# Performance work log

Hardware: AMD Instinct MI355X
Metric: run time of the kernel (lower is better)

Reference implementation:

```python
import jax, jax.numpy as jnp
import numpy as np

B, T, E, H, C = 64, 512, 512, 1024, 32
FORGET_BIAS = 1.0


def setup_inputs() -> dict:
    key = jax.random.key(0)
    ks = jax.random.split(key, 6)
    x = jax.random.normal(ks[0], (B, T, E), dtype=jnp.float32)
    # one-hot labels (softmax_cross_entropy_with_logits expects a distribution)
    y_idx = jax.random.randint(ks[1], (B,), 0, C)
    y = jax.nn.one_hot(y_idx, C, dtype=jnp.float32)
    seqlen = jnp.full((B,), T, dtype=jnp.int32)  # unused by dynamic_rnn in source
    # BasicLSTMCell kernel: concat([x, h]) @ W + b, gates split as i, j, f, o
    W = jax.random.normal(ks[2], (E + H, 4 * H), dtype=jnp.float32) * 0.02
    b = jnp.zeros((4 * H,), dtype=jnp.float32)
    out_W = jax.random.normal(ks[3], (H, C), dtype=jnp.float32)
    out_b = jax.random.normal(ks[4], (C,), dtype=jnp.float32)
    return {"x": x, "y": y, "seqlen": seqlen, "W": W, "b": b,
            "out_W": out_W, "out_b": out_b}


def lstm_last_output(x, W, b):
    # x: [B, T, E]; returns h_T: [B, H] (== outputs[:, -1] of dynamic_rnn)
    Bn = x.shape[0]
    Hn = W.shape[1] // 4

    def step(carry, xt):
        c, h = carry
        gates = jnp.concatenate([xt, h], axis=1) @ W + b  # [B, 4H]
        i, j, f, o = jnp.split(gates, 4, axis=1)
        new_c = c * jax.nn.sigmoid(f + FORGET_BIAS) + jax.nn.sigmoid(i) * jnp.tanh(j)
        new_h = jnp.tanh(new_c) * jax.nn.sigmoid(o)
        return (new_c, new_h), None

    init = (jnp.zeros((Bn, Hn), x.dtype), jnp.zeros((Bn, Hn), x.dtype))
    (_, h_last), _ = jax.lax.scan(step, init, jnp.swapaxes(x, 0, 1))  # scan over T
    return h_last


def reference(x, y, seqlen, W, b, out_W, out_b):
    h_last = lstm_last_output(x, W, b)
    pred = h_last @ out_W + out_b                    # logits [B, C]
    pred_softmax = jax.nn.softmax(pred, axis=-1)
    log_p = jax.nn.log_softmax(pred, axis=-1)
    cost = jnp.mean(-jnp.sum(y * log_p, axis=-1))    # mean softmax CE
    return pred, pred_softmax, cost
```

## Files before the change

### kernel.cpp

```cpp
#include <hip/hip_runtime.h>
#include <hip/hip_bf16.h>


#define Bb 64
#define Tt 512
#define Ee 512
#define Hh 1024
#define Cc 32
#define G4 4096
#define NKS 48
#define NBLK 128
#define HIDB 8
#define FPAD 32
#define NREP 16

typedef __attribute__((ext_vector_type(8))) short short8;
typedef __attribute__((ext_vector_type(4))) float f32x4;

__device__ __forceinline__ unsigned short f2bf(float f) {
  __hip_bfloat16 h = __float2bfloat16(f);
  union { __hip_bfloat16 h; unsigned short u; } cv; cv.h = h; return cv.u;
}
static __device__ __forceinline__ float fsig(float x) { return 1.0f / (1.0f + __expf(-x)); }
static __device__ __forceinline__ float ftanhf(float x) {
  float e = __expf(-2.0f * fabsf(x));
  float t = (1.0f - e) / (1.0f + e);
  return copysignf(t, x);
}

__global__ __launch_bounds__(256) void transpose_x_kernel(const float* __restrict__ x,
                                                          unsigned short* __restrict__ xT) {
  const int bid = blockIdx.x;
  const int row = bid >> 9, t = bid & (Tt - 1);
  const int e = threadIdx.x * 2;
  const float* src = x + ((size_t)row * Tt + t) * Ee + e;
  float2 v = *(const float2*)src;
  ushort2 o; o.x = f2bf(v.x); o.y = f2bf(v.y);
  *(ushort2*)(xT + ((size_t)t * Bb + row) * Ee + e) = o;
}

__global__ __launch_bounds__(64) void pack_w_kernel(const float* __restrict__ W,
                                                    unsigned short* __restrict__ Wpk) {
  const int fid = blockIdx.x;
  const int l = threadIdx.x;
  const int blk = fid / 96, rem = fid % 96;
  const int tau = rem / 48, ks = rem % 48;
  const int c = l & 15;
  const int col = (2 * tau + (c >> 3)) * Hh + blk * HIDB + (c & 7);
  const int k0 = ks * 32 + (l >> 4) * 8;
  short8 v;
#pragma unroll
  for (int i = 0; i < 8; i++) v[i] = (short)f2bf(W[(size_t)(k0 + i) * G4 + col]);
  *(short8*)(Wpk + ((size_t)fid * 64 + l) * 8) = v;
}

__global__ __launch_bounds__(256) void init_state_kernel(unsigned short* __restrict__ h0,
                                                         int* __restrict__ flg) {
  int i = blockIdx.x * 256 + threadIdx.x;
  h0[i] = 0;
  if (i < 4 * NBLK * FPAD + 4 * NREP * FPAD) flg[i] = 0;
}

__global__ __launch_bounds__(256, 1) void lstm_persist(
    const unsigned short* __restrict__ xT, const unsigned short* __restrict__ Wpk,
    const float* __restrict__ bias,
    unsigned short* __restrict__ hseq,
    float* __restrict__ h_f32, int* __restrict__ flg) {
  const int bc = blockIdx.x;
  const int tid = threadIdx.x;
  const int wv = tid >> 6, ln = tid & 63;

  int* epoch = flg + 4 * NBLK * FPAD;

  if (bc == NBLK) {
    int* flgw2 = flg + wv * NBLK * FPAD;
    int* ep = epoch + wv * NREP * FPAD;
    int cur = 0;
    while (cur < Tt - 1) {
      int a = __hip_atomic_load(flgw2 + ln * FPAD,        __ATOMIC_RELAXED, __HIP_MEMORY_SCOPE_AGENT);
      int b = __hip_atomic_load(flgw2 + (ln + 64) * FPAD, __ATOMIC_RELAXED, __HIP_MEMORY_SCOPE_AGENT);
      int m = a < b ? a : b;
#pragma unroll
      for (int off = 32; off >= 1; off >>= 1) {
        int o = __shfl_xor(m, off);
        m = o < m ? o : m;
      }
      if (m > cur) {
        cur = m;
        if (ln < NREP)
          __hip_atomic_store(ep + ln * FPAD, cur, __ATOMIC_RELAXED, __HIP_MEMORY_SCOPE_AGENT);
      }
    }
    return;
  }

  __shared__ short8 Wl[2 * NKS * 64];

  {
    const short8* src = (const short8*)Wpk + (size_t)bc * (2 * NKS * 64);
    for (int i = tid; i < 2 * NKS * 64; i += 256) Wl[i] = src[i];
  }

  const int c = ln & 15, kg = ln >> 4;
  const int arow = wv * 16 + c;
  const int rbase = wv * 16 + kg * 4;
  const int hid = bc * HIDB + (c & 7);
  const bool lo = (c < 8);
  const float bi = bias[hid], bj = bias[Hh + hid];
  const float bff = bias[2 * Hh + hid], bo = bias[3 * Hh + hid];
  float cstate[4] = {0.f, 0.f, 0.f, 0.f};

  __syncthreads();

  const short8* W0 = Wl;
  const short8* W1 = Wl + NKS * 64;

  short8 wx0[16], wx1[16];
#pragma unroll
  for (int kk = 0; kk < 16; kk++) { wx0[kk] = W0[kk * 64 + ln]; wx1[kk] = W1[kk * 64 + ln]; }

  int* flgw = flg + wv * NBLK * FPAD;
  int* myslot = flgw + bc * FPAD;
  int* myep = epoch + (wv * NREP + (bc & (NREP - 1))) * FPAD;

  f32x4 xa0, xa1;
  {
    const unsigned short* xr = xT + ((size_t)0 * Bb + arow) * Ee + kg * 8;
    f32x4 a0 = {0.f,0.f,0.f,0.f}, a1 = {0.f,0.f,0.f,0.f};
#pragma unroll
    for (int kk = 0; kk < 16; kk++) {
      short8 a = *(const short8*)(xr + kk * 32);
      a0 = __builtin_amdgcn_mfma_f32_16x16x32_bf16(a, wx0[kk], a0, 0, 0, 0);
      a1 = __builtin_amdgcn_mfma_f32_16x16x32_bf16(a, wx1[kk], a1, 0, 0, 0);
    }
    xa0 = a0; xa1 = a1;
  }

  for (int t = 0; t < Tt; t++) {
    while (__hip_atomic_load(myep, __ATOMIC_RELAXED, __HIP_MEMORY_SCOPE_AGENT) < t) { }
    asm volatile("" ::: "memory");

    const unsigned short* hr = hseq + (size_t)t * (NBLK * Bb * HIDB) + kg * 512 + arow * 8;
    short8 f[32];
#pragma unroll
    for (int kk = 0; kk < 32; kk++) f[kk] = *(const short8*)(hr + kk * 2048);
    asm volatile("s_waitcnt vmcnt(16)" ::: "memory");
    __builtin_amdgcn_sched_barrier(0);

    f32x4 a0 = xa0, a1 = xa1;
#pragma unroll
    for (int kk = 0; kk < 16; kk++) {
      a0 = __builtin_amdgcn_mfma_f32_16x16x32_bf16(f[kk], W0[(16 + kk) * 64 + ln], a0, 0, 0, 0);
      a1 = __builtin_amdgcn_mfma_f32_16x16x32_bf16(f[kk], W1[(16 + kk) * 64 + ln], a1, 0, 0, 0);
    }
    asm volatile("s_waitcnt vmcnt(0)" ::: "memory");
    __builtin_amdgcn_sched_barrier(0);
#pragma unroll
    for (int kk = 16; kk < 32; kk++) {
      a0 = __builtin_amdgcn_mfma_f32_16x16x32_bf16(f[kk], W0[(16 + kk) * 64 + ln], a0, 0, 0, 0);
      a1 = __builtin_amdgcn_mfma_f32_16x16x32_bf16(f[kk], W1[(16 + kk) * 64 + ln], a1, 0, 0, 0);
    }

    if (t < Tt - 1) {
      unsigned long long* hob = (unsigned long long*)hseq
                                + (size_t)(t + 1) * (NBLK * Bb * HIDB / 4)
                                + bc * (Bb * HIDB / 4);
#pragma unroll
      for (int r = 0; r < 4; r++) {
        const float p0 = a0[r], p1 = a1[r];
        const float s0 = __shfl_xor(p0, 8), s1 = __shfl_xor(p1, 8);
        const float gi = (lo ? p0 : s0) + bi;
        const float gj = (lo ? s0 : p0) + bj;
        const float gf = (lo ? p1 : s1) + bff;
        const float go = (lo ? s1 : p1) + bo;
        const float cn = cstate[r] * fsig(gf + 1.0f) + fsig(gi) * ftanhf(gj);
        cstate[r] = cn;
        const float hn = ftanhf(cn) * fsig(go);
        unsigned short us = f2bf(hn);
        unsigned short ps = (unsigned short)__shfl_xor((int)us, 1);
        unsigned int hw = (unsigned)us | ((unsigned)ps << 16);
        unsigned int p2 = (unsigned)__shfl_xor((int)hw, 2);
        unsigned long long hq = (unsigned long long)hw | ((unsigned long long)p2 << 32);
        if (lo && !(c & 3))
          __hip_atomic_store(hob + (rbase + r) * 2 + (c >> 2),
                             hq, __ATOMIC_RELAXED, __HIP_MEMORY_SCOPE_AGENT);
      }
      asm volatile("" ::: "memory");
      const unsigned short* xr = xT + ((size_t)(t + 1) * Bb + arow) * Ee + kg * 8;
      short8 xl[16];
#pragma unroll
      for (int kk = 0; kk < 16; kk++) xl[kk] = *(const short8*)(xr + kk * 32);
      asm volatile("s_waitcnt vmcnt(16)" ::: "memory");
      __builtin_amdgcn_sched_barrier(0);
      if (ln == 0)
        __hip_atomic_store(myslot, t + 1, __ATOMIC_RELAXED, __HIP_MEMORY_SCOPE_AGENT);
      {
        f32x4 b0 = {0.f,0.f,0.f,0.f}, b1 = {0.f,0.f,0.f,0.f};
#pragma unroll
        for (int kk = 0; kk < 16; kk++) {
          b0 = __builtin_amdgcn_mfma_f32_16x16x32_bf16(xl[kk], wx0[kk], b0, 0, 0, 0);
          b1 = __builtin_amdgcn_mfma_f32_16x16x32_bf16(xl[kk], wx1[kk], b1, 0, 0, 0);
        }
        xa0 = b0; xa1 = b1;
      }
    } else {
      float hnew[4];
#pragma unroll
      for (int r = 0; r < 4; r++) {
        const float p0 = a0[r], p1 = a1[r];
        const float s0 = __shfl_xor(p0, 8), s1 = __shfl_xor(p1, 8);
        const float gi = (lo ? p0 : s0) + bi;
        const float gj = (lo ? s0 : p0) + bj;
        const float gf = (lo ? p1 : s1) + bff;
        const float go = (lo ? s1 : p1) + bo;
        const float cn = cstate[r] * fsig(gf + 1.0f) + fsig(gi) * ftanhf(gj);
        cstate[r] = cn;
        hnew[r] = ftanhf(cn) * fsig(go);
      }
      if (lo) {
#pragma unroll
        for (int r = 0; r < 4; r++) h_f32[(rbase + r) * Hh + hid] = hnew[r];
      }
    }
  }
}

__global__ __launch_bounds__(256) void classifier_kernel(
    const float* __restrict__ h, const float* __restrict__ outW,
    const float* __restrict__ outb, const float* __restrict__ y,
    float* __restrict__ out, float* __restrict__ losses) {
  __shared__ float red[256];
  const int brow = blockIdx.x;
  const int tid = threadIdx.x;
  const int cc = tid & 31;
  const int part = tid >> 5;
  const float* hr = h + brow * Hh;
  float p = 0.f;
  for (int k = part * 128; k < part * 128 + 128; k++)
    p += hr[k] * outW[k * Cc + cc];
  red[tid] = p;
  __syncthreads();
  if (part < 4) red[tid] += red[tid + 128];
  __syncthreads();
  if (part < 2) red[tid] += red[tid + 64];
  __syncthreads();
  if (part < 1) red[tid] += red[tid + 32];
  __syncthreads();
  if (tid < 32) {
    const float logit = red[tid] + outb[tid];
    float m = logit;
    for (int off = 16; off >= 1; off >>= 1) m = fmaxf(m, __shfl_xor(m, off));
    const float e = __expf(logit - m);
    float s = e;
    for (int off = 16; off >= 1; off >>= 1) s += __shfl_xor(s, off);
    out[brow * Cc + tid] = logit;
    out[Bb * Cc + brow * Cc + tid] = e / s;
    const float logp = (logit - m) - __logf(s);
    float contrib = y[brow * Cc + tid] * logp;
    for (int off = 16; off >= 1; off >>= 1) contrib += __shfl_xor(contrib, off);
    if (tid == 0) losses[brow] = -contrib;
  }
}

__global__ __launch_bounds__(64) void finalize_kernel(const float* __restrict__ losses,
                                                      float* __restrict__ out) {
  float v = losses[threadIdx.x];
  for (int off = 32; off >= 1; off >>= 1) v += __shfl_down(v, off);
  if (threadIdx.x == 0) out[2 * Bb * Cc] = v * (1.0f / Bb);
}

extern "C" void kernel_launch(void* const* d_in, const int* in_sizes, int n_in,
                              void* d_out, int out_size, void* d_ws, size_t ws_size,
                              hipStream_t stream) {
  const float* x    = (const float*)d_in[0];
  const float* y    = (const float*)d_in[1];
  const float* W    = (const float*)d_in[3];
  const float* bias = (const float*)d_in[4];
  const float* outW = (const float*)d_in[5];
  const float* outb = (const float*)d_in[6];
  float* out = (float*)d_out;

  char* wsp = (char*)d_ws;
  size_t off = 0;
  auto walloc = [&](size_t bytes) -> void* {
    void* p = wsp + off;
    off += (bytes + 255) & ~(size_t)255;
    return p;
  };
  unsigned short* xT   = (unsigned short*)walloc((size_t)Bb * Tt * Ee * 2);
  unsigned short* Wpk  = (unsigned short*)walloc((size_t)NBLK * 2 * NKS * 64 * 16);
  unsigned short* hseq = (unsigned short*)walloc((size_t)Tt * Bb * Hh * 2);
  float* hf     = (float*)walloc((size_t)Bb * Hh * 4);
  float* losses = (float*)walloc(256);
  int* flg      = (int*)walloc((4 * NBLK * FPAD + 4 * NREP * FPAD) * 4);
  (void)ws_size; (void)in_sizes; (void)n_in; (void)out_size;

  transpose_x_kernel<<<Bb * Tt, 256, 0, stream>>>(x, xT);
  pack_w_kernel<<<NBLK * 2 * NKS, 64, 0, stream>>>(W, Wpk);
  init_state_kernel<<<(Bb * Hh) / 256, 256, 0, stream>>>(hseq, flg);

  lstm_persist<<<NBLK + 1, 256, 0, stream>>>(xT, Wpk, bias, hseq, hf, flg);

  classifier_kernel<<<Bb, 256, 0, stream>>>(hf, outW, outb, y, out, losses);
  finalize_kernel<<<1, 64, 0, stream>>>(losses, out);
}
```

Baseline: 3.089 ms.

## Replace global step barrier with per-group readiness flags and overlapped h loads

The single aggregator block that waited for all 128 producer blocks before publishing one epoch is replaced by two aggregator blocks. Each publishes a per-group readiness counter covering 16 producer blocks. Consumer blocks now wait group by group, loading that group's h slice and running its MFMAs while later groups are still finishing, so the wait overlaps compute instead of sitting behind a full barrier. The change adds more polling traffic, an extra spinning block, and a second accumulator pair that must be summed at the end.

```diff
diff --git a/kernel.cpp b/kernel.cpp
--- a/kernel.cpp
+++ b/kernel.cpp
@@ -72,24 +72,33 @@
 
   int* epoch = flg + 4 * NBLK * FPAD;
 
-  if (bc == NBLK) {
+  if (bc >= NBLK) {
+    const int ag = bc - NBLK;
     int* flgw2 = flg + wv * NBLK * FPAD;
-    int* ep = epoch + wv * NREP * FPAD;
+    int* ep = epoch + (wv * NREP + ag * 8) * FPAD;
+    const int gidx = ln >> 3;
+    int prevg = 0;
     int cur = 0;
     while (cur < Tt - 1) {
-      int a = __hip_atomic_load(flgw2 + ln * FPAD,        __ATOMIC_RELAXED, __HIP_MEMORY_SCOPE_AGENT);
-      int b = __hip_atomic_load(flgw2 + (ln + 64) * FPAD, __ATOMIC_RELAXED, __HIP_MEMORY_SCOPE_AGENT);
+      int a = __hip_atomic_load(flgw2 + (2 * ln) * FPAD,     __ATOMIC_RELAXED, __HIP_MEMORY_SCOPE_AGENT);
+      int b = __hip_atomic_load(flgw2 + (2 * ln + 1) * FPAD, __ATOMIC_RELAXED, __HIP_MEMORY_SCOPE_AGENT);
       int m = a < b ? a : b;
 #pragma unroll
-      for (int off = 32; off >= 1; off >>= 1) {
+      for (int off = 1; off <= 4; off <<= 1) {
         int o = __shfl_xor(m, off);
         m = o < m ? o : m;
       }
-      if (m > cur) {
-        cur = m;
-        if (ln < NREP)
-          __hip_atomic_store(ep + ln * FPAD, cur, __ATOMIC_RELAXED, __HIP_MEMORY_SCOPE_AGENT);
-      }
+      if ((ln & 7) == 0 && m > prevg) {
+        __hip_atomic_store(ep + gidx * FPAD, m, __ATOMIC_RELAXED, __HIP_MEMORY_SCOPE_AGENT);
+        prevg = m;
+      }
+      int fm = m;
+#pragma unroll
+      for (int off = 8; off <= 32; off <<= 1) {
+        int o = __shfl_xor(fm, off);
+        fm = o < fm ? o : fm;
+      }
+      cur = fm;
     }
     return;
   }
@@ -121,7 +130,8 @@
 
   int* flgw = flg + wv * NBLK * FPAD;
   int* myslot = flgw + bc * FPAD;
-  int* myep = epoch + (wv * NREP + (bc & (NREP - 1))) * FPAD;
+  int* epA = epoch + (wv * NREP) * FPAD;
+  int* epB = epoch + (wv * NREP + 8) * FPAD;
 
   f32x4 xa0, xa1;
   {
@@ -136,30 +146,54 @@
     xa0 = a0; xa1 = a1;
   }
 
+#define POLLG(G) do {                                                          \
+    pe0 = __hip_atomic_load(epA + (G) * FPAD, __ATOMIC_RELAXED, __HIP_MEMORY_SCOPE_AGENT); \
+    pe1 = __hip_atomic_load(epB + (G) * FPAD, __ATOMIC_RELAXED, __HIP_MEMORY_SCOPE_AGENT); \
+    __builtin_amdgcn_sched_barrier(0x187);                                     \
+  } while (0)
+
+#define WAITG(G) do {                                                          \
+    while (pe0 < t && pe1 < t) {                                               \
+      pe0 = __hip_atomic_load(epA + (G) * FPAD, __ATOMIC_RELAXED, __HIP_MEMORY_SCOPE_AGENT); \
+      pe1 = __hip_atomic_load(epB + (G) * FPAD, __ATOMIC_RELAXED, __HIP_MEMORY_SCOPE_AGENT); \
+    }                                                                          \
+    asm volatile("" ::: "memory");                                             \
+  } while (0)
+
+#define LOADG(G) do {                                                          \
+    f[4*(G)+0] = *(const short8*)(hr + (4*(G)+0) * 2048);                      \
+    f[4*(G)+1] = *(const short8*)(hr + (4*(G)+1) * 2048);                      \
+    f[4*(G)+2] = *(const short8*)(hr + (4*(G)+2) * 2048);                      \
+    f[4*(G)+3] = *(const short8*)(hr + (4*(G)+3) * 2048);                      \
+    __builtin_amdgcn_sched_barrier(0x187);                                     \
+  } while (0)
+
+#define MFMAG(G, A0, A1) do {                                                  \
+    _Pragma("unroll")                                                          \
+    for (int kk = 4*(G); kk < 4*(G)+4; kk++) {                                 \
+      A0 = __builtin_amdgcn_mfma_f32_16x16x32_bf16(f[kk], W0[(16+kk)*64+ln], A0, 0, 0, 0); \
+      A1 = __builtin_amdgcn_mfma_f32_16x16x32_bf16(f[kk], W1[(16+kk)*64+ln], A1, 0, 0, 0); \
+    }                                                                          \
+  } while (0)
+
   for (int t = 0; t < Tt; t++) {
-    while (__hip_atomic_load(myep, __ATOMIC_RELAXED, __HIP_MEMORY_SCOPE_AGENT) < t) { }
-    asm volatile("" ::: "memory");
-
     const unsigned short* hr = hseq + (size_t)t * (NBLK * Bb * HIDB) + kg * 512 + arow * 8;
     short8 f[32];
-#pragma unroll
-    for (int kk = 0; kk < 32; kk++) f[kk] = *(const short8*)(hr + kk * 2048);
-    asm volatile("s_waitcnt vmcnt(16)" ::: "memory");
-    __builtin_amdgcn_sched_barrier(0);
-
     f32x4 a0 = xa0, a1 = xa1;
-#pragma unroll
-    for (int kk = 0; kk < 16; kk++) {
-      a0 = __builtin_amdgcn_mfma_f32_16x16x32_bf16(f[kk], W0[(16 + kk) * 64 + ln], a0, 0, 0, 0);
-      a1 = __builtin_amdgcn_mfma_f32_16x16x32_bf16(f[kk], W1[(16 + kk) * 64 + ln], a1, 0, 0, 0);
-    }
-    asm volatile("s_waitcnt vmcnt(0)" ::: "memory");
-    __builtin_amdgcn_sched_barrier(0);
-#pragma unroll
-    for (int kk = 16; kk < 32; kk++) {
-      a0 = __builtin_amdgcn_mfma_f32_16x16x32_bf16(f[kk], W0[(16 + kk) * 64 + ln], a0, 0, 0, 0);
-      a1 = __builtin_amdgcn_mfma_f32_16x16x32_bf16(f[kk], W1[(16 + kk) * 64 + ln], a1, 0, 0, 0);
-    }
+    f32x4 b0 = {0.f,0.f,0.f,0.f}, b1 = {0.f,0.f,0.f,0.f};
+    int pe0, pe1;
+
+    POLLG(0);
+    WAITG(0); POLLG(1); LOADG(0);
+    WAITG(1); POLLG(2); LOADG(1); MFMAG(0, a0, a1);
+    WAITG(2); POLLG(3); LOADG(2); MFMAG(1, a0, a1);
+    WAITG(3); POLLG(4); LOADG(3); MFMAG(2, a0, a1);
+    WAITG(4); POLLG(5); LOADG(4); MFMAG(3, a0, a1);
+    WAITG(5); POLLG(6); LOADG(5); MFMAG(4, b0, b1);
+    WAITG(6); POLLG(7); LOADG(6); MFMAG(5, b0, b1);
+    WAITG(7);           LOADG(7); MFMAG(6, b0, b1);
+    MFMAG(7, b0, b1);
+    a0 += b0; a1 += b1;
 
     if (t < Tt - 1) {
       unsigned long long* hob = (unsigned long long*)hseq
@@ -191,17 +225,17 @@
 #pragma unroll
       for (int kk = 0; kk < 16; kk++) xl[kk] = *(const short8*)(xr + kk * 32);
       asm volatile("s_waitcnt vmcnt(16)" ::: "memory");
-      __builtin_amdgcn_sched_barrier(0);
+      __builtin_amdgcn_sched_barrier(0x187);
       if (ln == 0)
         __hip_atomic_store(myslot, t + 1, __ATOMIC_RELAXED, __HIP_MEMORY_SCOPE_AGENT);
       {
-        f32x4 b0 = {0.f,0.f,0.f,0.f}, b1 = {0.f,0.f,0.f,0.f};
+        f32x4 c0 = {0.f,0.f,0.f,0.f}, c1 = {0.f,0.f,0.f,0.f};
 #pragma unroll
         for (int kk = 0; kk < 16; kk++) {
-          b0 = __builtin_amdgcn_mfma_f32_16x16x32_bf16(xl[kk], wx0[kk], b0, 0, 0, 0);
-          b1 = __builtin_amdgcn_mfma_f32_16x16x32_bf16(xl[kk], wx1[kk], b1, 0, 0, 0);
+          c0 = __builtin_amdgcn_mfma_f32_16x16x32_bf16(xl[kk], wx0[kk], c0, 0, 0, 0);
+          c1 = __builtin_amdgcn_mfma_f32_16x16x32_bf16(xl[kk], wx1[kk], c1, 0, 0, 0);
         }
-        xa0 = b0; xa1 = b1;
+        xa0 = c0; xa1 = c1;
       }
     } else {
       float hnew[4];
@@ -223,6 +257,10 @@
       }
     }
   }
+#undef POLLG
+#undef WAITG
+#undef LOADG
+#undef MFMAG
 }
 
 __global__ __launch_bounds__(256) void classifier_kernel(
@@ -299,7 +337,7 @@
   pack_w_kernel<<<NBLK * 2 * NKS, 64, 0, stream>>>(W, Wpk);
   init_state_kernel<<<(Bb * Hh) / 256, 256, 0, stream>>>(hseq, flg);
 
-  lstm_persist<<<NBLK + 1, 256, 0, stream>>>(xT, Wpk, bias, hseq, hf, flg);
+  lstm_persist<<<NBLK + 2, 256, 0, stream>>>(xT, Wpk, bias, hseq, hf, flg);
 
   classifier_kernel<<<Bb, 256, 0, stream>>>(hf, outW, outb, y, out, losses);
   finalize_kernel<<<1, 64, 0, stream>>>(losses, out);
```

New measurement: 3.469 ms. 1.12x slower.
